# Performance work log

Hardware: AMD Instinct MI355X
Metric: run time of the kernel (lower is better)

The kernel has to match this reference:

```python
import jax, jax.numpy as jnp
import numpy as np

B, INPUTDIM, OUTDIM, GRIDSIZE = 4096, 128, 512, 300

def setup_inputs() -> dict:
    key = jax.random.key(0)
    k1, k2 = jax.random.split(key)
    x = jax.random.normal(k1, (B, INPUTDIM), dtype=jnp.float32)
    scale = 1.0 / (np.sqrt(INPUTDIM) * np.sqrt(GRIDSIZE))
    fouriercoeffs = jax.random.normal(k2, (2, OUTDIM, INPUTDIM, GRIDSIZE), dtype=jnp.float32) * scale
    return {"x": x, "fouriercoeffs": fouriercoeffs}

def reference(x, fouriercoeffs):
    # k: frequencies 1..gridsize
    gridsize = fouriercoeffs.shape[-1]
    k = jnp.arange(1, gridsize + 1, dtype=x.dtype)  # (G,)
    arg = x[:, :, None] * k  # (B, I, G)
    c = jnp.cos(arg)
    s = jnp.sin(arg)
    # einsum('dbik,djik->bj') with d=2 split into cos/sin terms
    y = jnp.einsum('big,jig->bj', c, fouriercoeffs[0]) + jnp.einsum('big,jig->bj', s, fouriercoeffs[1])
    return y
```

## Files before the change

kernel.cpp:

```cpp
#include <hip/hip_runtime.h>
#include <hip/hip_bf16.h>
#include <cstdint>

#define TB 256
#define TBG 512

typedef short short8 __attribute__((ext_vector_type(8)));
typedef float f32x4 __attribute__((ext_vector_type(4)));

constexpr int B_N = 4096, I_N = 128, J_N = 512, G_N = 300;
constexpr int K1 = I_N * G_N;
constexpr int BM = 128, BN = 512;
constexpr int NSP = 8;
constexpr int IC = 16;
constexpr float INV2PI = 0.15915494309189535f;

constexpr int GSTRIDE = 4 * 512 * 8;
constexpr size_t SPSTRIDE = (size_t)G_N * GSTRIDE;

__device__ __forceinline__ ushort f2bf(float f) {
    unsigned int u = __float_as_uint(f);
    return (ushort)((u + 0x7FFFu + ((u >> 16) & 1u)) >> 16);
}

__device__ __forceinline__ float fract_(float x) {
#if __has_builtin(__builtin_amdgcn_fractf)
    return __builtin_amdgcn_fractf(x);
#else
    return x - floorf(x);
#endif
}

__device__ __forceinline__ unsigned int pack_bf2(float a, float b) {
    __hip_bfloat162 h = __float22bfloat162_rn(make_float2(a, b));
    unsigned int u;
    __builtin_memcpy(&u, &h, 4);
    return u;
}

typedef __attribute__((address_space(3))) unsigned int lds_u32_t;
typedef __attribute__((address_space(1))) const unsigned int glb_u32_t;

__device__ __forceinline__ void llds16(const void* g, void* l) {
    __builtin_amdgcn_global_load_lds(
        reinterpret_cast<glb_u32_t*>(reinterpret_cast<uintptr_t>(g)),
        reinterpret_cast<lds_u32_t*>((unsigned int)reinterpret_cast<uintptr_t>(l)),
        16, 0, 0);
}

constexpr int TRG = 60;
constexpr int TRTB = 512;
constexpr int TRUNITS = 256 * 15;

__global__ __launch_bounds__(TRTB) void fkan_tr(const float* __restrict__ src,
                                                ushort* __restrict__ dst,
                                                float* __restrict__ outz) {
    __shared__ __align__(16) ushort L[TRG * 2 * 32 * 8];
    const int gc = blockIdx.x;
    const int sp = blockIdx.y;
    const int djc = blockIdx.z;
    const int dj0 = djc * 32;
    const int d = dj0 >> 9;
    const int j0 = dj0 & 511;
    const int g0 = gc * TRG;
    const int tid = threadIdx.x;

    {
        size_t bid = (size_t)(djc * 8 + sp) * 5 + gc;
        size_t zt = bid * TRTB + tid;
        if (zt < (size_t)B_N * J_N / 4)
            ((float4*)outz)[zt] = make_float4(0.f, 0.f, 0.f, 0.f);
    }

    unsigned int* Lw = (unsigned int*)L;

    auto rbody = [&](int u) {
        int rp = u / 15, c = u - rp * 15;
        int djl = rp >> 3, ilp = rp & 7;
        int ihl = ilp >> 2, e2 = ilp & 3;
        const float* p = src + ((size_t)(dj0 + djl) * 128 + sp * 16 + ilp * 2) * 300
                       + g0 + c * 4;
        float4 va = *(const float4*)p;
        float4 vb = *(const float4*)(p + 300);
        float a[4] = {va.x, va.y, va.z, va.w};
        float b[4] = {vb.x, vb.y, vb.z, vb.w};
        const int swz = (c & 7) << 2;
#pragma unroll
        for (int k = 0; k < 4; ++k) {
            int gl = c * 4 + k;
            int wd = ((gl * 2 + ihl) * 32 + djl) * 4 + e2;
            Lw[wd ^ swz] = pack_bf2(a[k], b[k]);
        }
    };
#pragma unroll
    for (int it = 0; it < 7; ++it) rbody(tid + it * TRTB);
    if (tid < TRUNITS - 7 * TRTB) rbody(tid + 7 * TRTB);
    __syncthreads();

    const uint4* Lv = (const uint4*)L;
    auto wbody = [&](int w) {
        int gl = w >> 6, r = w & 63;
        int ihl = r >> 5, jl = r & 31;
        int q = (gl * 64 + ihl * 32 + jl) ^ ((gl >> 2) & 7);
        size_t d16 = ((size_t)(sp * G_N + g0 + gl) * 4 + d * 2 + ihl) * 512 + j0 + jl;
        ((uint4*)dst)[d16] = Lv[q];
    };
#pragma unroll
    for (int it = 0; it < 7; ++it) wbody(tid + it * TRTB);
    if (tid < TRG * 64 - 7 * TRTB) wbody(tid + 7 * TRTB);
}

__global__ __launch_bounds__(TBG, 2)
void fkan_gemm(const float* __restrict__ x,
               const ushort* __restrict__ fcb,
               float* __restrict__ out) {
    __shared__ __align__(16) ushort At[2 * 4 * 128 * 8];

    const int tid = threadIdx.x;
    const int bm = blockIdx.x, sp = blockIdx.z;
    const int lane = tid & 63, wid = tid >> 6;
    const int lhi = lane >> 4, llo = lane & 15;

    const int m = tid >> 2;
    const int q4 = tid & 3;
    const int ihq = q4 >> 1, eq = (q4 & 1) * 4;

    float sv[4], cv[4], s0[4], c0[4];
    {
        const float* xr = x + ((size_t)(bm * BM + m)) * I_N + sp * IC + q4 * 4;
        float4 xa = *(const float4*)xr;
        float xv[4] = {xa.x, xa.y, xa.z, xa.w};
#pragma unroll
        for (int j = 0; j < 4; ++j) {
            float r = fract_(xv[j] * INV2PI);
            s0[j] = __builtin_amdgcn_sinf(r);
            c0[j] = __builtin_amdgcn_cosf(r);
            sv[j] = s0[j];
            cv[j] = c0[j];
        }
    }

    ushort* awc0 = &At[(ihq * 128 + m) * 8 + eq];
    ushort* aws0 = &At[((2 + ihq) * 128 + m) * 8 + eq];

    const ushort* bbase = fcb + (size_t)sp * SPSTRIDE
                        + ((size_t)lhi * 512 + wid * 64 + llo) * 8;
    auto loadB = [&](short8* br, int g) {
        const ushort* p = bbase + (size_t)g * GSTRIDE;
#pragma unroll
        for (int t = 0; t < 4; ++t)
            br[t] = *(const short8*)(p + t * 128);
    };

    const int aoff = (lhi * 128 + llo) * 8;

    f32x4 acc[8][4];
#pragma unroll
    for (int a = 0; a < 8; ++a)
#pragma unroll
        for (int b = 0; b < 4; ++b) acc[a][b] = (f32x4){0.f, 0.f, 0.f, 0.f};

    auto writeA = [&](int nb) {
        uint2 vc = {pack_bf2(cv[0], cv[1]), pack_bf2(cv[2], cv[3])};
        *(uint2*)(awc0 + nb * 4096) = vc;
        uint2 vs = {pack_bf2(sv[0], sv[1]), pack_bf2(sv[2], sv[3])};
        *(uint2*)(aws0 + nb * 4096) = vs;
#pragma unroll
        for (int j = 0; j < 4; ++j) {
            float t = __builtin_fmaf(sv[j], c0[j], cv[j] * s0[j]);
            cv[j] = __builtin_fmaf(cv[j], c0[j], -(sv[j] * s0[j]));
            sv[j] = t;
        }
    };

    short8 bA[4], bB[4];

    auto halfstep = [&](int cb, short8* bcur, short8* bnxt, int gnext, bool doNext) {
        __syncthreads();
        if (doNext) loadB(bnxt, gnext);
        short8 af[8];
#pragma unroll
        for (int t = 0; t < 8; ++t)
            af[t] = *(const short8*)&At[cb * 4096 + aoff + t * 128];
#pragma unroll
        for (int tm = 0; tm < 8; ++tm)
#pragma unroll
            for (int tn = 0; tn < 4; ++tn)
                acc[tm][tn] = __builtin_amdgcn_mfma_f32_16x16x32_bf16(
                    af[tm], bcur[tn], acc[tm][tn], 0, 0, 0);
        if (doNext) writeA(cb ^ 1);
    };

    writeA(0);
    loadB(bA, 0);

    for (int g = 0; g < G_N; g += 2) {
        halfstep(0, bA, bB, g + 1, true);
        halfstep(1, bB, bA, g + 2, g + 2 < G_N);
    }

    const int row0 = bm * BM + lhi * 4;
    const int col0 = wid * 64 + llo;
#pragma unroll
    for (int tm = 0; tm < 8; ++tm)
#pragma unroll
        for (int tn = 0; tn < 4; ++tn)
#pragma unroll
            for (int r = 0; r < 4; ++r)
                atomicAdd(&out[(size_t)(row0 + tm * 16 + r) * J_N + col0 + tn * 16],
                          acc[tm][tn][r]);
}

constexpr int SPL_FB = 4;
constexpr int KS_FB = 2 * K1 / SPL_FB;
constexpr int NSTEP_FB = KS_FB / 32;

__global__ __launch_bounds__(TB)
void fkan_gemm_fb(const float* __restrict__ x,
                  const float* __restrict__ fc32,
                  float* __restrict__ out) {
    __shared__ float xs[128][65];
    __shared__ __align__(16) ushort At[4 * 128 * 8];
    __shared__ __align__(16) ushort Bt[4 * 128 * 8];

    const int tid = threadIdx.x;
    const int bm = blockIdx.x, bn = blockIdx.y, sp = blockIdx.z;
    const int d = sp >> 1;
    const int ib = (sp & 1) << 6;
    const int rbase = ib * G_N;

    for (int idx = tid; idx < 128 * 64; idx += TB) {
        int row = idx >> 6, il = idx & 63;
        xs[row][il] = x[(size_t)(bm * 128 + row) * I_N + ib + il];
    }

    f32x4 acc[4][4];
#pragma unroll
    for (int a = 0; a < 4; ++a)
#pragma unroll
        for (int b = 0; b < 4; ++b) acc[a][b] = (f32x4){0.f, 0.f, 0.f, 0.f};

    const int lane = tid & 63, wid = tid >> 6;
    const int wm = wid & 1, wn = wid >> 1;
    const int lhi = lane >> 4, llo = lane & 15;
    const int am = tid & 127, akg0 = tid >> 7;

    const float* f32base = fc32 + ((size_t)d * J_N + bn * 128) * K1 + rbase;

    for (int step = 0; step < NSTEP_FB; ++step) {
        __syncthreads();
#pragma unroll
        for (int it = 0; it < 2; ++it) {
            const int kg = akg0 + it * 2;
            int r = rbase + step * 32 + kg * 8;
            int i = (int)((unsigned)r / 300u);
            int g = r - i * 300;
            float xxv = xs[am][i - ib];
            float kkf = (float)(g + 1);
            short8 avv;
#pragma unroll
            for (int j = 0; j < 8; ++j) {
                float rev = xxv * kkf * INV2PI;
                float fr = fract_(rev) + (d ? 0.0f : 0.25f);
                avv[j] = (short)f2bf(__builtin_amdgcn_sinf(fract_(fr)));
                if (j < 7) {
                    ++g; kkf += 1.0f;
                    if (g == 300) { g = 0; kkf = 1.0f; ++i; xxv = xs[am][i - ib]; }
                }
            }
            *(short8*)&At[(kg * 128 + am) * 8] = avv;
        }
#pragma unroll
        for (int it = 0; it < 2; ++it) {
            int item = tid + it * TB;
            int n = item >> 2, grp = item & 3;
            const float* gp = f32base + (size_t)n * K1 + step * 32 + grp * 8;
            float4 v0 = *(const float4*)gp;
            float4 v1 = *(const float4*)(gp + 4);
            short8 bv;
            bv[0] = (short)f2bf(v0.x); bv[1] = (short)f2bf(v0.y);
            bv[2] = (short)f2bf(v0.z); bv[3] = (short)f2bf(v0.w);
            bv[4] = (short)f2bf(v1.x); bv[5] = (short)f2bf(v1.y);
            bv[6] = (short)f2bf(v1.z); bv[7] = (short)f2bf(v1.w);
            *(short8*)&Bt[(grp * 128 + n) * 8] = bv;
        }
        __syncthreads();
        short8 af[4], bf[4];
#pragma unroll
        for (int t = 0; t < 4; ++t) {
            af[t] = *(const short8*)&At[(lhi * 128 + wm * 64 + t * 16 + llo) * 8];
            bf[t] = *(const short8*)&Bt[(lhi * 128 + wn * 64 + t * 16 + llo) * 8];
        }
#pragma unroll
        for (int tm = 0; tm < 4; ++tm)
#pragma unroll
            for (int tn = 0; tn < 4; ++tn)
                acc[tm][tn] = __builtin_amdgcn_mfma_f32_16x16x32_bf16(
                    af[tm], bf[tn], acc[tm][tn], 0, 0, 0);
    }

    const int row0 = bm * 128 + wm * 64 + lhi * 4;
    const int col0 = bn * 128 + wn * 64 + llo;
#pragma unroll
    for (int tm = 0; tm < 4; ++tm)
#pragma unroll
        for (int tn = 0; tn < 4; ++tn)
#pragma unroll
            for (int r = 0; r < 4; ++r)
                atomicAdd(&out[(size_t)(row0 + tm * 16 + r) * J_N + col0 + tn * 16],
                          acc[tm][tn][r]);
}

extern "C" void kernel_launch(void* const* d_in, const int* in_sizes, int n_in,
                              void* d_out, int out_size, void* d_ws, size_t ws_size,
                              hipStream_t stream) {
    const float* x = (const float*)d_in[0];
    const float* fc = (const float*)d_in[1];
    float* out = (float*)d_out;

    const size_t need = (size_t)2 * J_N * K1 * sizeof(ushort);

    if (ws_size >= need) {
        ushort* fcb = (ushort*)d_ws;
        fkan_tr<<<dim3(5, 8, 32), TRTB, 0, stream>>>(fc, fcb, out);
        dim3 grid(B_N / BM, 1, NSP);
        fkan_gemm<<<grid, TBG, 0, stream>>>(x, fcb, out);
    } else {
        hipMemsetAsync(d_out, 0, (size_t)out_size * sizeof(float), stream);
        dim3 grid(B_N / 128, J_N / 128, SPL_FB);
        fkan_gemm_fb<<<grid, TB, 0, stream>>>(x, fc, out);
    }
}
```

Baseline: 529.6 us.

## Process two grid frequencies per barrier with doubled LDS A buffers

The main GEMM loop now stages two frequency slices of the cos/sin A tile per LDS buffer, so only one __syncthreads is needed per two frequencies instead of one per frequency. B fragments for both frequencies are prefetched into registers and reloaded right after each MFMA block consumes them. This doubles LDS usage for A and changes when B loads are issued, which may affect occupancy, register pressure and how well loads overlap with compute.

```diff
diff --git a/kernel.cpp b/kernel.cpp
--- a/kernel.cpp
+++ b/kernel.cpp
@@ -114,7 +114,7 @@
 void fkan_gemm(const float* __restrict__ x,
                const ushort* __restrict__ fcb,
                float* __restrict__ out) {
-    __shared__ __align__(16) ushort At[2 * 4 * 128 * 8];
+    __shared__ __align__(16) ushort At[2 * 8 * 128 * 8];
 
     const int tid = threadIdx.x;
     const int bm = blockIdx.x, sp = blockIdx.z;
@@ -160,11 +160,11 @@
 #pragma unroll
         for (int b = 0; b < 4; ++b) acc[a][b] = (f32x4){0.f, 0.f, 0.f, 0.f};
 
-    auto writeA = [&](int nb) {
+    auto putA = [&](int nb, int pr) {
         uint2 vc = {pack_bf2(cv[0], cv[1]), pack_bf2(cv[2], cv[3])};
-        *(uint2*)(awc0 + nb * 4096) = vc;
+        *(uint2*)(awc0 + nb * 8192 + pr * 4096) = vc;
         uint2 vs = {pack_bf2(sv[0], sv[1]), pack_bf2(sv[2], sv[3])};
-        *(uint2*)(aws0 + nb * 4096) = vs;
+        *(uint2*)(aws0 + nb * 8192 + pr * 4096) = vs;
 #pragma unroll
         for (int j = 0; j < 4; ++j) {
             float t = __builtin_fmaf(sv[j], c0[j], cv[j] * s0[j]);
@@ -173,30 +173,43 @@
         }
     };
 
-    short8 bA[4], bB[4];
-
-    auto halfstep = [&](int cb, short8* bcur, short8* bnxt, int gnext, bool doNext) {
+    short8 b0[4], b1[4];
+
+    putA(0, 0);
+    putA(0, 1);
+    loadB(b0, 0);
+    loadB(b1, 1);
+
+    for (int iv = 0; iv < G_N / 2; ++iv) {
+        const int cb = iv & 1;
+        const int gb = iv * 2;
+        const bool more = iv < G_N / 2 - 1;
         __syncthreads();
-        if (doNext) loadB(bnxt, gnext);
         short8 af[8];
 #pragma unroll
         for (int t = 0; t < 8; ++t)
-            af[t] = *(const short8*)&At[cb * 4096 + aoff + t * 128];
+            af[t] = *(const short8*)&At[cb * 8192 + aoff + t * 128];
 #pragma unroll
         for (int tm = 0; tm < 8; ++tm)
 #pragma unroll
             for (int tn = 0; tn < 4; ++tn)
                 acc[tm][tn] = __builtin_amdgcn_mfma_f32_16x16x32_bf16(
-                    af[tm], bcur[tn], acc[tm][tn], 0, 0, 0);
-        if (doNext) writeA(cb ^ 1);
-    };
-
-    writeA(0);
-    loadB(bA, 0);
-
-    for (int g = 0; g < G_N; g += 2) {
-        halfstep(0, bA, bB, g + 1, true);
-        halfstep(1, bB, bA, g + 2, g + 2 < G_N);
+                    af[tm], b0[tn], acc[tm][tn], 0, 0, 0);
+        if (more) loadB(b0, gb + 2);
+#pragma unroll
+        for (int t = 0; t < 8; ++t)
+            af[t] = *(const short8*)&At[cb * 8192 + 4096 + aoff + t * 128];
+#pragma unroll
+        for (int tm = 0; tm < 8; ++tm)
+#pragma unroll
+            for (int tn = 0; tn < 4; ++tn)
+                acc[tm][tn] = __builtin_amdgcn_mfma_f32_16x16x32_bf16(
+                    af[tm], b1[tn], acc[tm][tn], 0, 0, 0);
+        if (more) {
+            loadB(b1, gb + 3);
+            putA(cb ^ 1, 0);
+            putA(cb ^ 1, 1);
+        }
     }
 
     const int row0 = bm * BM + lhi * 4;
```

Result: faster. 512.7 us (-3.2%).
